# Kernel optimization log

Hardware: AMD Instinct MI355X
Metric: run time of the kernel (lower is better)

The kernel has to match this reference:

```python
import jax, jax.numpy as jnp
import numpy as np

B, F, L, D = 256, 4, 64, 768
HID = (F + F) * 200  # 1600
NEG = -1e10


def setup_inputs() -> dict:
    key = jax.random.key(0)
    ks = jax.random.split(key, 8)
    left = jax.random.normal(ks[0], (B, F, L, D), dtype=jnp.float32)
    right = jax.random.normal(ks[1], (B, F, L, D), dtype=jnp.float32)
    # emulate ragged padding: last quarter of tokens are zero (masked out)
    left = left.at[:, :, 3 * L // 4 :, :].set(0.0)
    right = right.at[:, :, 3 * L // 4 :, :].set(0.0)
    femb_l = jax.random.normal(ks[2], (F, D), dtype=jnp.float32)
    femb_r = jax.random.normal(ks[3], (F, D), dtype=jnp.float32)
    empty_attr = jax.random.normal(ks[4], (D,), dtype=jnp.float32) * 0.05
    in_dim = 2 * F * D
    W1 = jax.random.normal(ks[5], (HID, in_dim), dtype=jnp.float32) * (1.0 / np.sqrt(in_dim))
    b1 = jnp.zeros((HID,), dtype=jnp.float32)
    W2 = jax.random.normal(ks[6], (2, HID), dtype=jnp.float32) * (1.0 / np.sqrt(HID))
    b2 = jnp.full((2,), -np.log((1 - 0.01) / 0.01), dtype=jnp.float32)
    return {"left": left, "right": right, "femb_l": femb_l, "femb_r": femb_r,
            "empty_attr": empty_attr, "W1": W1, "b1": b1, "W2": W2, "b2": b2}


def _attribute_matching(v, femb, empty_attr):
    # v: [B, F, L, D], femb: [F, D]
    tok_mask = (v != 0).sum(axis=-1) > 0          # [B, F, L]
    attr_mask = tok_mask.any(axis=-1)              # [B, F]
    logits = jnp.einsum('bfld,fd->bfl', v, femb)   # per-field attention scores
    logits = logits + jnp.where(tok_mask, 0.0, NEG)
    w = jax.nn.softmax(logits, axis=2)             # masked softmax over tokens
    summary = jnp.einsum('bfl,bfld->bfd', w, v)    # attention pooling
    return jnp.where(attr_mask[..., None], summary, empty_attr)  # [B, F, D]


def reference(left, right, femb_l, femb_r, empty_attr, W1, b1, W2, b2):
    l_rep = _attribute_matching(left, femb_l, empty_attr)
    r_rep = _attribute_matching(right, femb_r, empty_attr)
    concat = jnp.concatenate([l_rep, r_rep], axis=1).reshape(left.shape[0], -1)
    h = jax.nn.relu(concat @ W1.T + b1)
    return h @ W2.T + b2  # [B, 2]
```

## Files before the change

kernel.cpp:

```cpp
#include <hip/hip_runtime.h>

typedef __attribute__((ext_vector_type(8))) short short8;
typedef __attribute__((ext_vector_type(4))) short short4_t;
typedef __attribute__((ext_vector_type(4))) float f32x4;

#define NEGBIG -1e10f

__device__ __forceinline__ unsigned short f2bf(float x) {
  unsigned int u = __float_as_uint(x);
  u += 0x7FFFu + ((u >> 16) & 1u);
  return (unsigned short)(u >> 16);
}
__device__ __forceinline__ unsigned pack2(float a, float b) {
  unsigned ua = __float_as_uint(a), ub = __float_as_uint(b);
  ua += 0x7FFFu + ((ua >> 16) & 1u);
  ub += 0x7FFFu + ((ub >> 16) & 1u);
  return (ua >> 16) | (ub & 0xFFFF0000u);
}
__device__ __forceinline__ float lo_bf(unsigned p) { return __uint_as_float(p << 16); }
__device__ __forceinline__ float hi_bf(unsigned p) { return __uint_as_float(p & 0xFFFF0000u); }
__device__ __forceinline__ float bfu(unsigned short h) { return __uint_as_float(((unsigned)h) << 16); }

__device__ __forceinline__ float4 mul4(float4 a, float s) {
  float4 r; r.x = a.x*s; r.y = a.y*s; r.z = a.z*s; r.w = a.w*s; return r;
}
__device__ __forceinline__ float4 add4(float4 a, float4 b) {
  float4 r; r.x = a.x+b.x; r.y = a.y+b.y; r.z = a.z+b.z; r.w = a.w+b.w; return r;
}

__global__ __launch_bounds__(256, 4) void pool_partial(
    const float* __restrict__ left, const float* __restrict__ right,
    const float* __restrict__ femb_l, const float* __restrict__ femb_r,
    unsigned short* __restrict__ partials,
    float4* __restrict__ meta)
{
  int bid     = blockIdx.x;
  int panel   = bid >> 2;
  int quarter = bid & 3;
  int side    = panel >> 10;
  int rem     = panel & 1023;
  int f       = rem & 3;
  const float* v    = (side ? right : left) + (size_t)rem * 64 * 768 + (size_t)quarter * 16 * 768;
  const float* femb = (side ? femb_r : femb_l) + f * 768;

  int tid = threadIdx.x, wave = tid >> 6, lane = tid & 63;

  const float4* fp = (const float4*)femb;
  float4 f0 = fp[lane], f1 = fp[lane + 64], f2 = fp[lane + 128];

  const float4* vp = (const float4*)(v + (size_t)wave * 4 * 768);

  float d[4];
  unsigned pk[4][6];
  unsigned nzmask = 0;

  #pragma unroll
  for (int g = 0; g < 2; ++g) {
    const float4* ta = vp + (g * 2 + 0) * 192 + lane;
    const float4* tb = vp + (g * 2 + 1) * 192 + lane;
    float4 xa0 = ta[0], xa1 = ta[64], xa2 = ta[128];
    float4 xb0 = tb[0], xb1 = tb[64], xb2 = tb[128];

    int t0 = g * 2, t1 = g * 2 + 1;
    d[t0] = xa0.x*f0.x + xa0.y*f0.y + xa0.z*f0.z + xa0.w*f0.w
          + xa1.x*f1.x + xa1.y*f1.y + xa1.z*f1.z + xa1.w*f1.w
          + xa2.x*f2.x + xa2.y*f2.y + xa2.z*f2.z + xa2.w*f2.w;
    unsigned nza = __float_as_uint(xa0.x) | __float_as_uint(xa0.y)
                 | __float_as_uint(xa0.z) | __float_as_uint(xa0.w)
                 | __float_as_uint(xa1.x) | __float_as_uint(xa1.y)
                 | __float_as_uint(xa1.z) | __float_as_uint(xa1.w)
                 | __float_as_uint(xa2.x) | __float_as_uint(xa2.y)
                 | __float_as_uint(xa2.z) | __float_as_uint(xa2.w);
    nzmask |= (nza != 0u) ? (1u << t0) : 0u;
    pk[t0][0] = pack2(xa0.x, xa0.y); pk[t0][1] = pack2(xa0.z, xa0.w);
    pk[t0][2] = pack2(xa1.x, xa1.y); pk[t0][3] = pack2(xa1.z, xa1.w);
    pk[t0][4] = pack2(xa2.x, xa2.y); pk[t0][5] = pack2(xa2.z, xa2.w);

    d[t1] = xb0.x*f0.x + xb0.y*f0.y + xb0.z*f0.z + xb0.w*f0.w
          + xb1.x*f1.x + xb1.y*f1.y + xb1.z*f1.z + xb1.w*f1.w
          + xb2.x*f2.x + xb2.y*f2.y + xb2.z*f2.z + xb2.w*f2.w;
    unsigned nzb = __float_as_uint(xb0.x) | __float_as_uint(xb0.y)
                 | __float_as_uint(xb0.z) | __float_as_uint(xb0.w)
                 | __float_as_uint(xb1.x) | __float_as_uint(xb1.y)
                 | __float_as_uint(xb1.z) | __float_as_uint(xb1.w)
                 | __float_as_uint(xb2.x) | __float_as_uint(xb2.y)
                 | __float_as_uint(xb2.z) | __float_as_uint(xb2.w);
    nzmask |= (nzb != 0u) ? (1u << t1) : 0u;
    pk[t1][0] = pack2(xb0.x, xb0.y); pk[t1][1] = pack2(xb0.z, xb0.w);
    pk[t1][2] = pack2(xb1.x, xb1.y); pk[t1][3] = pack2(xb1.z, xb1.w);
    pk[t1][4] = pack2(xb2.x, xb2.y); pk[t1][5] = pack2(xb2.z, xb2.w);
  }

  #pragma unroll
  for (int sh = 32; sh > 0; sh >>= 1) {
    d[0] += __shfl_xor(d[0], sh);
    d[1] += __shfl_xor(d[1], sh);
    d[2] += __shfl_xor(d[2], sh);
    d[3] += __shfl_xor(d[3], sh);
    nzmask |= __shfl_xor(nzmask, sh);
  }

  float l[4], e[4];
  #pragma unroll
  for (int t = 0; t < 4; ++t)
    l[t] = d[t] + (((nzmask >> t) & 1u) ? 0.f : NEGBIG);
  float m_w = fmaxf(fmaxf(l[0], l[1]), fmaxf(l[2], l[3]));
  #pragma unroll
  for (int t = 0; t < 4; ++t) e[t] = __expf(l[t] - m_w);
  float s_w = (e[0] + e[1]) + (e[2] + e[3]);

  __shared__ float m_lds[4], s_lds[4];
  __shared__ int   nz_lds[4];
  __shared__ float acc_lds[4 * 768];

  if (lane == 0) { m_lds[wave] = m_w; s_lds[wave] = s_w; nz_lds[wave] = (nzmask != 0u); }

  float4 A0 = {0,0,0,0}, A1 = {0,0,0,0}, A2 = {0,0,0,0};
  #pragma unroll
  for (int t = 0; t < 4; ++t) {
    float c = e[t];
    A0.x += c * lo_bf(pk[t][0]); A0.y += c * hi_bf(pk[t][0]);
    A0.z += c * lo_bf(pk[t][1]); A0.w += c * hi_bf(pk[t][1]);
    A1.x += c * lo_bf(pk[t][2]); A1.y += c * hi_bf(pk[t][2]);
    A1.z += c * lo_bf(pk[t][3]); A1.w += c * hi_bf(pk[t][3]);
    A2.x += c * lo_bf(pk[t][4]); A2.y += c * hi_bf(pk[t][4]);
    A2.z += c * lo_bf(pk[t][5]); A2.w += c * hi_bf(pk[t][5]);
  }

  __syncthreads();
  float M = fmaxf(fmaxf(m_lds[0], m_lds[1]), fmaxf(m_lds[2], m_lds[3]));
  float S = s_lds[0] * __expf(m_lds[0] - M) + s_lds[1] * __expf(m_lds[1] - M)
          + s_lds[2] * __expf(m_lds[2] - M) + s_lds[3] * __expf(m_lds[3] - M);
  float scale = __expf(m_w - M);

  float4* al = (float4*)acc_lds;
  al[wave * 192 +       lane] = mul4(A0, scale);
  al[wave * 192 +  64 + lane] = mul4(A1, scale);
  al[wave * 192 + 128 + lane] = mul4(A2, scale);
  __syncthreads();

  if (tid < 192) {
    float4 A = add4(add4(al[tid], al[192 + tid]),
                    add4(al[384 + tid], al[576 + tid]));
    ushort4 o;
    o.x = f2bf(A.x); o.y = f2bf(A.y); o.z = f2bf(A.z); o.w = f2bf(A.w);
    ((ushort4*)(partials + (size_t)bid * 768))[tid] = o;
  }
  if (tid == 192) {
    int has = nz_lds[0] | nz_lds[1] | nz_lds[2] | nz_lds[3];
    float4 mt; mt.x = M; mt.y = S; mt.z = has ? 1.f : 0.f; mt.w = 0.f;
    meta[bid] = mt;
  }
}

__global__ __launch_bounds__(192) void pool_merge(
    const unsigned short* __restrict__ partials, const float4* __restrict__ meta,
    const float* __restrict__ empty_attr,
    unsigned short* __restrict__ concat)
{
  int panel = blockIdx.x;
  int tid = threadIdx.x;
  int side = panel >> 10;
  int rem  = panel & 1023;
  int f    = rem & 3;
  int b    = rem >> 2;

  int p4 = panel * 4;
  float4 mt0 = meta[p4], mt1 = meta[p4 + 1], mt2 = meta[p4 + 2], mt3 = meta[p4 + 3];
  float M = fmaxf(fmaxf(mt0.x, mt1.x), fmaxf(mt2.x, mt3.x));
  float sc0 = __expf(mt0.x - M), sc1 = __expf(mt1.x - M);
  float sc2 = __expf(mt2.x - M), sc3 = __expf(mt3.x - M);
  float S = mt0.y * sc0 + mt1.y * sc1 + mt2.y * sc2 + mt3.y * sc3;
  int has = (mt0.z + mt1.z + mt2.z + mt3.z) != 0.f;

  ushort4 q0 = ((const ushort4*)(partials + (size_t)(p4 + 0) * 768))[tid];
  ushort4 q1 = ((const ushort4*)(partials + (size_t)(p4 + 1) * 768))[tid];
  ushort4 q2 = ((const ushort4*)(partials + (size_t)(p4 + 2) * 768))[tid];
  ushort4 q3 = ((const ushort4*)(partials + (size_t)(p4 + 3) * 768))[tid];

  float4 r;
  if (has) {
    float i0 = sc0 / S, i1 = sc1 / S, i2 = sc2 / S, i3 = sc3 / S;
    r.x = bfu(q0.x)*i0 + bfu(q1.x)*i1 + bfu(q2.x)*i2 + bfu(q3.x)*i3;
    r.y = bfu(q0.y)*i0 + bfu(q1.y)*i1 + bfu(q2.y)*i2 + bfu(q3.y)*i3;
    r.z = bfu(q0.z)*i0 + bfu(q1.z)*i1 + bfu(q2.z)*i2 + bfu(q3.z)*i3;
    r.w = bfu(q0.w)*i0 + bfu(q1.w)*i1 + bfu(q2.w)*i2 + bfu(q3.w)*i3;
  } else {
    r = ((const float4*)empty_attr)[tid];
  }
  ushort4 o;
  o.x = f2bf(r.x); o.y = f2bf(r.y); o.z = f2bf(r.z); o.w = f2bf(r.w);
  size_t base = ((size_t)b * 8 + side * 4 + f) * 192;
  ((ushort4*)concat)[base + tid] = o;
}

__global__ __launch_bounds__(256) void gemm1_kernel(
    const unsigned short* __restrict__ A,
    const float* __restrict__ W1,
    float* __restrict__ Hpart)
{
  const int K = 6144, N = 1600, KC = 768;
  int colb = blockIdx.x;
  int kc   = blockIdx.y;
  int col0 = colb * 16;
  int tid = threadIdx.x, wave = tid >> 6, lane = tid & 63;

  __shared__ short wlds[96 * 16 * 8];

  const float* wsrc = W1 + (size_t)col0 * K + kc * KC;
  #pragma unroll
  for (int i = 0; i < 12; ++i) {
    int flat4 = tid + 256 * i;
    int col = flat4 / 192;
    int k   = (flat4 % 192) * 4;
    float4 w = *(const float4*)(wsrc + (size_t)col * K + k);
    short4_t o;
    o[0] = (short)f2bf(w.x); o[1] = (short)f2bf(w.y);
    o[2] = (short)f2bf(w.z); o[3] = (short)f2bf(w.w);
    *(short4_t*)(wlds + (k >> 3) * 128 + col * 8 + (k & 7)) = o;
  }
  __syncthreads();

  int lr = lane & 15;
  const short* a0 = (const short*)A + (size_t)(wave * 64 + lr) * K + kc * KC + (lane >> 4) * 8;
  const short* bptr = wlds + (lane >> 4) * 128 + lr * 8;

  f32x4 acc0 = {}, acc1 = {}, acc2 = {}, acc3 = {};

  #pragma unroll 4
  for (int ks = 0; ks < 24; ++ks) {
    short8 bf  = *(const short8*)(bptr + ks * 512);
    short8 af0 = *(const short8*)(a0 + ks * 32);
    short8 af1 = *(const short8*)(a0 + ks * 32 + 16 * K);
    short8 af2 = *(const short8*)(a0 + ks * 32 + 32 * K);
    short8 af3 = *(const short8*)(a0 + ks * 32 + 48 * K);
    acc0 = __builtin_amdgcn_mfma_f32_16x16x32_bf16(af0, bf, acc0, 0, 0, 0);
    acc1 = __builtin_amdgcn_mfma_f32_16x16x32_bf16(af1, bf, acc1, 0, 0, 0);
    acc2 = __builtin_amdgcn_mfma_f32_16x16x32_bf16(af2, bf, acc2, 0, 0, 0);
    acc3 = __builtin_amdgcn_mfma_f32_16x16x32_bf16(af3, bf, acc3, 0, 0, 0);
  }

  int ccol = lane & 15;
  int crow = (lane >> 4) * 4;
  float* hp = Hpart + (size_t)kc * 256 * N + (size_t)col0 + ccol;
  f32x4 accs[4] = {acc0, acc1, acc2, acc3};
  #pragma unroll
  for (int i = 0; i < 4; ++i) {
    int r = wave * 64 + i * 16 + crow;
    #pragma unroll
    for (int q = 0; q < 4; ++q)
      hp[(size_t)(r + q) * N] = accs[i][q];
  }
}

__global__ __launch_bounds__(256) void epilogue_kernel(
    const float* __restrict__ Hpart, const float* __restrict__ b1,
    const float* __restrict__ W2, const float* __restrict__ b2,
    float* __restrict__ out)
{
  const int N = 1600;
  int b = blockIdx.x, tid = threadIdx.x;
  int wave = tid >> 6, lane = tid & 63;
  float s0 = 0.f, s1 = 0.f;
  for (int c = tid; c < N; c += 256) {
    float acc = 0.f;
    #pragma unroll
    for (int kc = 0; kc < 8; ++kc)
      acc += Hpart[((size_t)kc * 256 + b) * N + c];
    float h = fmaxf(acc + b1[c], 0.f);
    s0 += h * W2[c];
    s1 += h * W2[N + c];
  }
  #pragma unroll
  for (int s = 32; s > 0; s >>= 1) {
    s0 += __shfl_xor(s0, s);
    s1 += __shfl_xor(s1, s);
  }
  __shared__ float r0[4], r1[4];
  if (lane == 0) { r0[wave] = s0; r1[wave] = s1; }
  __syncthreads();
  if (tid == 0) {
    out[b * 2 + 0] = r0[0] + r0[1] + r0[2] + r0[3] + b2[0];
    out[b * 2 + 1] = r1[0] + r1[1] + r1[2] + r1[3] + b2[1];
  }
}

extern "C" void kernel_launch(void* const* d_in, const int* in_sizes, int n_in,
                              void* d_out, int out_size, void* d_ws, size_t ws_size,
                              hipStream_t stream) {
  const float* left       = (const float*)d_in[0];
  const float* right      = (const float*)d_in[1];
  const float* femb_l     = (const float*)d_in[2];
  const float* femb_r     = (const float*)d_in[3];
  const float* empty_attr = (const float*)d_in[4];
  const float* W1         = (const float*)d_in[5];
  const float* b1         = (const float*)d_in[6];
  const float* W2         = (const float*)d_in[7];
  const float* b2         = (const float*)d_in[8];
  float* out = (float*)d_out;

  char* ws = (char*)d_ws;
  unsigned short* concat = (unsigned short*)ws;
  float*          Hpart  = (float*)(ws + 3145728);
  unsigned short* partials = (unsigned short*)Hpart;
  float4*         meta     = (float4*)(ws + 3145728 + 12582912);

  hipLaunchKernelGGL(pool_partial, dim3(8192), dim3(256), 0, stream,
                     left, right, femb_l, femb_r, partials, meta);
  hipLaunchKernelGGL(pool_merge, dim3(2048), dim3(192), 0, stream,
                     partials, meta, empty_attr, concat);
  hipLaunchKernelGGL(gemm1_kernel, dim3(100, 8), dim3(256), 0, stream,
                     concat, W1, Hpart);
  hipLaunchKernelGGL(epilogue_kernel, dim3(256), dim3(256), 0, stream,
                     Hpart, b1, W2, b2, out);
}
```

Before: 139.6 us.

## Stage pooling panel in LDS via direct global-to-LDS loads

The partial pooling kernel now copies its 16x768 float token panel straight into shared memory with global_load_lds, instead of keeping bf16-packed copies in registers. Logits are computed from LDS, and the 16 logits are shared through LDS so each thread can do the softmax weighting and sum over all tokens from the LDS panel. This removes the bf16 pack/unpack and the per-wave rescale-and-reduce pass, and accumulates in full fp32. In exchange each block now uses about 48KB of LDS, the launch-bounds occupancy hint is dropped, and 64 threads sit idle during accumulation, so fewer blocks may fit per CU.

After: 138.0 us. About the same (-1.1%).

```diff
diff --git a/kernel.cpp b/kernel.cpp
--- a/kernel.cpp
+++ b/kernel.cpp
@@ -11,14 +11,6 @@
   u += 0x7FFFu + ((u >> 16) & 1u);
   return (unsigned short)(u >> 16);
 }
-__device__ __forceinline__ unsigned pack2(float a, float b) {
-  unsigned ua = __float_as_uint(a), ub = __float_as_uint(b);
-  ua += 0x7FFFu + ((ua >> 16) & 1u);
-  ub += 0x7FFFu + ((ub >> 16) & 1u);
-  return (ua >> 16) | (ub & 0xFFFF0000u);
-}
-__device__ __forceinline__ float lo_bf(unsigned p) { return __uint_as_float(p << 16); }
-__device__ __forceinline__ float hi_bf(unsigned p) { return __uint_as_float(p & 0xFFFF0000u); }
 __device__ __forceinline__ float bfu(unsigned short h) { return __uint_as_float(((unsigned)h) << 16); }
 
 __device__ __forceinline__ float4 mul4(float4 a, float s) {
@@ -28,7 +20,14 @@
   float4 r; r.x = a.x+b.x; r.y = a.y+b.y; r.z = a.z+b.z; r.w = a.w+b.w; return r;
 }
 
-__global__ __launch_bounds__(256, 4) void pool_partial(
+__device__ __forceinline__ void g2l16(const float* g, float* l) {
+  __builtin_amdgcn_global_load_lds(
+      (const __attribute__((address_space(1))) void*)g,
+      (__attribute__((address_space(3))) void*)l,
+      16, 0, 0);
+}
+
+__global__ __launch_bounds__(256) void pool_partial(
     const float* __restrict__ left, const float* __restrict__ right,
     const float* __restrict__ femb_l, const float* __restrict__ femb_r,
     unsigned short* __restrict__ partials,
@@ -45,52 +44,42 @@
 
   int tid = threadIdx.x, wave = tid >> 6, lane = tid & 63;
 
+  __shared__ float    panel_lds[16 * 768];
+  __shared__ float    l_lds[16];
+  __shared__ unsigned nz_lds[4];
+
   const float4* fp = (const float4*)femb;
   float4 f0 = fp[lane], f1 = fp[lane + 64], f2 = fp[lane + 128];
 
-  const float4* vp = (const float4*)(v + (size_t)wave * 4 * 768);
-
+  const float* vw = v + (size_t)wave * 4 * 768;
+  float*       lw = panel_lds + wave * 4 * 768;
+  #pragma unroll
+  for (int t = 0; t < 4; ++t) {
+    #pragma unroll
+    for (int j = 0; j < 3; ++j)
+      g2l16(vw + t * 768 + j * 256 + lane * 4, lw + t * 768 + j * 256);
+  }
+  asm volatile("s_waitcnt vmcnt(0)" ::: "memory");
+
+  const float4* pw = (const float4*)lw;
   float d[4];
-  unsigned pk[4][6];
   unsigned nzmask = 0;
-
-  #pragma unroll
-  for (int g = 0; g < 2; ++g) {
-    const float4* ta = vp + (g * 2 + 0) * 192 + lane;
-    const float4* tb = vp + (g * 2 + 1) * 192 + lane;
-    float4 xa0 = ta[0], xa1 = ta[64], xa2 = ta[128];
-    float4 xb0 = tb[0], xb1 = tb[64], xb2 = tb[128];
-
-    int t0 = g * 2, t1 = g * 2 + 1;
-    d[t0] = xa0.x*f0.x + xa0.y*f0.y + xa0.z*f0.z + xa0.w*f0.w
-          + xa1.x*f1.x + xa1.y*f1.y + xa1.z*f1.z + xa1.w*f1.w
-          + xa2.x*f2.x + xa2.y*f2.y + xa2.z*f2.z + xa2.w*f2.w;
-    unsigned nza = __float_as_uint(xa0.x) | __float_as_uint(xa0.y)
-                 | __float_as_uint(xa0.z) | __float_as_uint(xa0.w)
-                 | __float_as_uint(xa1.x) | __float_as_uint(xa1.y)
-                 | __float_as_uint(xa1.z) | __float_as_uint(xa1.w)
-                 | __float_as_uint(xa2.x) | __float_as_uint(xa2.y)
-                 | __float_as_uint(xa2.z) | __float_as_uint(xa2.w);
-    nzmask |= (nza != 0u) ? (1u << t0) : 0u;
-    pk[t0][0] = pack2(xa0.x, xa0.y); pk[t0][1] = pack2(xa0.z, xa0.w);
-    pk[t0][2] = pack2(xa1.x, xa1.y); pk[t0][3] = pack2(xa1.z, xa1.w);
-    pk[t0][4] = pack2(xa2.x, xa2.y); pk[t0][5] = pack2(xa2.z, xa2.w);
-
-    d[t1] = xb0.x*f0.x + xb0.y*f0.y + xb0.z*f0.z + xb0.w*f0.w
-          + xb1.x*f1.x + xb1.y*f1.y + xb1.z*f1.z + xb1.w*f1.w
-          + xb2.x*f2.x + xb2.y*f2.y + xb2.z*f2.z + xb2.w*f2.w;
-    unsigned nzb = __float_as_uint(xb0.x) | __float_as_uint(xb0.y)
-                 | __float_as_uint(xb0.z) | __float_as_uint(xb0.w)
-                 | __float_as_uint(xb1.x) | __float_as_uint(xb1.y)
-                 | __float_as_uint(xb1.z) | __float_as_uint(xb1.w)
-                 | __float_as_uint(xb2.x) | __float_as_uint(xb2.y)
-                 | __float_as_uint(xb2.z) | __float_as_uint(xb2.w);
-    nzmask |= (nzb != 0u) ? (1u << t1) : 0u;
-    pk[t1][0] = pack2(xb0.x, xb0.y); pk[t1][1] = pack2(xb0.z, xb0.w);
-    pk[t1][2] = pack2(xb1.x, xb1.y); pk[t1][3] = pack2(xb1.z, xb1.w);
-    pk[t1][4] = pack2(xb2.x, xb2.y); pk[t1][5] = pack2(xb2.z, xb2.w);
-  }
-
+  #pragma unroll
+  for (int t = 0; t < 4; ++t) {
+    float4 x0 = pw[t * 192 + lane];
+    float4 x1 = pw[t * 192 + 64 + lane];
+    float4 x2 = pw[t * 192 + 128 + lane];
+    d[t] = x0.x*f0.x + x0.y*f0.y + x0.z*f0.z + x0.w*f0.w
+         + x1.x*f1.x + x1.y*f1.y + x1.z*f1.z + x1.w*f1.w
+         + x2.x*f2.x + x2.y*f2.y + x2.z*f2.z + x2.w*f2.w;
+    unsigned nzb = __float_as_uint(x0.x) | __float_as_uint(x0.y)
+                 | __float_as_uint(x0.z) | __float_as_uint(x0.w)
+                 | __float_as_uint(x1.x) | __float_as_uint(x1.y)
+                 | __float_as_uint(x1.z) | __float_as_uint(x1.w)
+                 | __float_as_uint(x2.x) | __float_as_uint(x2.y)
+                 | __float_as_uint(x2.z) | __float_as_uint(x2.w);
+    nzmask |= (nzb != 0u) ? (1u << t) : 0u;
+  }
   #pragma unroll
   for (int sh = 32; sh > 0; sh >>= 1) {
     d[0] += __shfl_xor(d[0], sh);
@@ -99,55 +88,39 @@
     d[3] += __shfl_xor(d[3], sh);
     nzmask |= __shfl_xor(nzmask, sh);
   }
-
-  float l[4], e[4];
-  #pragma unroll
-  for (int t = 0; t < 4; ++t)
-    l[t] = d[t] + (((nzmask >> t) & 1u) ? 0.f : NEGBIG);
-  float m_w = fmaxf(fmaxf(l[0], l[1]), fmaxf(l[2], l[3]));
-  #pragma unroll
-  for (int t = 0; t < 4; ++t) e[t] = __expf(l[t] - m_w);
-  float s_w = (e[0] + e[1]) + (e[2] + e[3]);
-
-  __shared__ float m_lds[4], s_lds[4];
-  __shared__ int   nz_lds[4];
-  __shared__ float acc_lds[4 * 768];
-
-  if (lane == 0) { m_lds[wave] = m_w; s_lds[wave] = s_w; nz_lds[wave] = (nzmask != 0u); }
-
-  float4 A0 = {0,0,0,0}, A1 = {0,0,0,0}, A2 = {0,0,0,0};
-  #pragma unroll
-  for (int t = 0; t < 4; ++t) {
-    float c = e[t];
-    A0.x += c * lo_bf(pk[t][0]); A0.y += c * hi_bf(pk[t][0]);
-    A0.z += c * lo_bf(pk[t][1]); A0.w += c * hi_bf(pk[t][1]);
-    A1.x += c * lo_bf(pk[t][2]); A1.y += c * hi_bf(pk[t][2]);
-    A1.z += c * lo_bf(pk[t][3]); A1.w += c * hi_bf(pk[t][3]);
-    A2.x += c * lo_bf(pk[t][4]); A2.y += c * hi_bf(pk[t][4]);
-    A2.z += c * lo_bf(pk[t][5]); A2.w += c * hi_bf(pk[t][5]);
-  }
-
+  if (lane == 0) {
+    #pragma unroll
+    for (int t = 0; t < 4; ++t)
+      l_lds[wave * 4 + t] = d[t] + (((nzmask >> t) & 1u) ? 0.f : NEGBIG);
+    nz_lds[wave] = nzmask & 0xFu;
+  }
   __syncthreads();
-  float M = fmaxf(fmaxf(m_lds[0], m_lds[1]), fmaxf(m_lds[2], m_lds[3]));
-  float S = s_lds[0] * __expf(m_lds[0] - M) + s_lds[1] * __expf(m_lds[1] - M)
-          + s_lds[2] * __expf(m_lds[2] - M) + s_lds[3] * __expf(m_lds[3] - M);
-  float scale = __expf(m_w - M);
-
-  float4* al = (float4*)acc_lds;
-  al[wave * 192 +       lane] = mul4(A0, scale);
-  al[wave * 192 +  64 + lane] = mul4(A1, scale);
-  al[wave * 192 + 128 + lane] = mul4(A2, scale);
-  __syncthreads();
+
+  float lv[16];
+  #pragma unroll
+  for (int t = 0; t < 16; ++t) lv[t] = l_lds[t];
+  float M = lv[0];
+  #pragma unroll
+  for (int t = 1; t < 16; ++t) M = fmaxf(M, lv[t]);
+  float e[16]; float S = 0.f;
+  #pragma unroll
+  for (int t = 0; t < 16; ++t) { e[t] = __expf(lv[t] - M); S += e[t]; }
+  unsigned has = nz_lds[0] | nz_lds[1] | nz_lds[2] | nz_lds[3];
 
   if (tid < 192) {
-    float4 A = add4(add4(al[tid], al[192 + tid]),
-                    add4(al[384 + tid], al[576 + tid]));
+    const float4* pf = (const float4*)panel_lds;
+    float4 acc = {0.f, 0.f, 0.f, 0.f};
+    #pragma unroll
+    for (int t = 0; t < 16; ++t) {
+      float4 x = pf[t * 192 + tid];
+      acc.x += e[t] * x.x; acc.y += e[t] * x.y;
+      acc.z += e[t] * x.z; acc.w += e[t] * x.w;
+    }
     ushort4 o;
-    o.x = f2bf(A.x); o.y = f2bf(A.y); o.z = f2bf(A.z); o.w = f2bf(A.w);
+    o.x = f2bf(acc.x); o.y = f2bf(acc.y); o.z = f2bf(acc.z); o.w = f2bf(acc.w);
     ((ushort4*)(partials + (size_t)bid * 768))[tid] = o;
   }
   if (tid == 192) {
-    int has = nz_lds[0] | nz_lds[1] | nz_lds[2] | nz_lds[3];
     float4 mt; mt.x = M; mt.y = S; mt.z = has ? 1.f : 0.f; mt.w = 0.f;
     meta[bid] = mt;
   }
```
